# Kernel tuning notes

Hardware: AMD Instinct MI355X
Metric: run time of the kernel (lower is better)

The kernel has to match this reference:

```python
import jax, jax.numpy as jnp
import numpy as np

B, S, H = 32, 2048, 1024

def setup_inputs() -> dict:
    key = jax.random.key(0)
    ks = jax.random.split(key, 8)
    s = 1.0 / np.sqrt(H)
    return {
        "query": jax.random.normal(ks[0], (B, 1, H), jnp.float32),
        "keys": jax.random.normal(ks[1], (B, S, H), jnp.float32),
        "Wa_w": jax.random.normal(ks[2], (H, H), jnp.float32) * s,
        "Wa_b": jax.random.normal(ks[3], (H,), jnp.float32) * s,
        "Ua_w": jax.random.normal(ks[4], (H, H), jnp.float32) * s,
        "Ua_b": jax.random.normal(ks[5], (H,), jnp.float32) * s,
        "Va_w": jax.random.normal(ks[6], (1, H), jnp.float32) * s,
        "Va_b": jax.random.normal(ks[7], (1,), jnp.float32) * s,
    }

def reference(query, keys, Wa_w, Wa_b, Ua_w, Ua_b, Va_w, Va_b):
    # Wa(query): (B,1,H); Ua(keys): (B,S,H); broadcast add -> (B,S,H)
    q = jnp.einsum('bqh,oh->bqo', query, Wa_w) + Wa_b
    k = jnp.einsum('bsh,oh->bso', keys, Ua_w) + Ua_b
    h = jnp.tanh(q + k)                              # (B,S,H)
    scores = jnp.einsum('bsh,oh->bso', h, Va_w) + Va_b  # (B,S,1)
    scores = scores[:, :, 0][:, None, :]             # (B,1,S)
    weights = jax.nn.softmax(scores, axis=-1)        # (B,1,S)
    context = jnp.einsum('bqs,bsh->bqh', weights, keys)  # (B,1,H)
    return context, weights
```

## Files before the change

kernel.cpp:

```cpp
#include <hip/hip_runtime.h>
#include <hip/hip_bf16.h>

#define HDIM 1024
#define SEQ  2048
#define BATCH 32
#define M_TOTAL (BATCH * SEQ)
#define BM 128
#define BN 256
#define BK 64
#define NSLICE 8

typedef __bf16 bf16x8 __attribute__((ext_vector_type(8)));
typedef float  f32x4  __attribute__((ext_vector_type(4)));
typedef unsigned short u16;
#define AS1 __attribute__((address_space(1)))
#define AS3 __attribute__((address_space(3)))

__device__ __forceinline__ u16 f2bf(float f) {
    unsigned int u = __float_as_uint(f);
    u += 0x7FFFu + ((u >> 16) & 1u);
    return (u16)(u >> 16);
}

__global__ __launch_bounds__(256) void cvt_kernel(const float* __restrict__ in,
                                                  u16* __restrict__ out) {
    size_t i = ((size_t)blockIdx.x * 256 + threadIdx.x) * 8;
    float4 f0 = *(const float4*)(in + i);
    float4 f1 = *(const float4*)(in + i + 4);
    uint4 v;
    v.x = (unsigned)f2bf(f0.x) | ((unsigned)f2bf(f0.y) << 16);
    v.y = (unsigned)f2bf(f0.z) | ((unsigned)f2bf(f0.w) << 16);
    v.z = (unsigned)f2bf(f1.x) | ((unsigned)f2bf(f1.y) << 16);
    v.w = (unsigned)f2bf(f1.z) | ((unsigned)f2bf(f1.w) << 16);
    *(uint4*)(out + i) = v;
}

__global__ __launch_bounds__(256) void qb_kernel(const float* __restrict__ query,
                                                 const float* __restrict__ Wa_w,
                                                 const float* __restrict__ Wa_b,
                                                 const float* __restrict__ Ua_b,
                                                 float* __restrict__ qb) {
    __shared__ float qs[HDIM];
    const int b = blockIdx.x;
    const int tid = threadIdx.x;
    ((float4*)qs)[tid] = ((const float4*)(query + b * HDIM))[tid];
    __syncthreads();
    const int lane = tid & 63;
    const int w = tid >> 6;
    const int obase = blockIdx.y * 64 + w * 16;
    for (int i = 0; i < 16; i++) {
        int o = obase + i;
        const float4* wrow = (const float4*)(Wa_w + (size_t)o * HDIM);
        float s = 0.f;
        #pragma unroll
        for (int j = 0; j < 4; j++) {
            float4 wv = wrow[j * 64 + lane];
            float4 qv = ((const float4*)qs)[j * 64 + lane];
            s += wv.x * qv.x + wv.y * qv.y + wv.z * qv.z + wv.w * qv.w;
        }
        #pragma unroll
        for (int m = 1; m < 64; m <<= 1) s += __shfl_xor(s, m);
        if (lane == 0) qb[b * HDIM + o] = s + Wa_b[o] + Ua_b[o];
    }
}

__global__ __launch_bounds__(256, 2) void gemm_score_kernel(const u16* __restrict__ keysb,
                                                            const u16* __restrict__ uab,
                                                            const float* __restrict__ qb,
                                                            const float* __restrict__ vaw,
                                                            float* __restrict__ sp) {
    __shared__ __align__(16) u16 As[BM * BK];
    __shared__ __align__(16) u16 Bs[BN * BK];
    const int tid  = threadIdx.x;
    const int lane = tid & 63;
    const int w    = tid >> 6;
    const int n0 = blockIdx.x * BN;
    const int m0 = blockIdx.y * BM;
    const int wave_m = (w & 1) * 64;
    const int wave_n = (w >> 1) * 128;

    f32x4 acc[4][8] = {};

    const int srow = lane >> 3;
    const int scol = (lane & 7) * 8;
    const u16* gA = keysb + (size_t)(m0 + w * 32 + srow) * HDIM + scol;
    const u16* gB = uab   + (size_t)(n0 + w * 64 + srow) * HDIM + scol;
    u16* lA = As + (w * 32) * BK;
    u16* lB = Bs + (w * 64) * BK;

    const int fr = lane & 15;
    const int fq = lane >> 4;

    for (int k0 = 0; k0 < HDIM; k0 += BK) {
        __syncthreads();
        #pragma unroll
        for (int i = 0; i < 4; i++)
            __builtin_amdgcn_global_load_lds((AS1 void*)(gA + k0 + i * 8 * HDIM),
                                             (AS3 void*)(lA + i * 8 * BK), 16, 0, 0);
        #pragma unroll
        for (int i = 0; i < 8; i++)
            __builtin_amdgcn_global_load_lds((AS1 void*)(gB + k0 + i * 8 * HDIM),
                                             (AS3 void*)(lB + i * 8 * BK), 16, 0, 0);
        __syncthreads();

        #pragma unroll
        for (int j = 0; j < 2; j++) {
            bf16x8 a[4], b[8];
            #pragma unroll
            for (int i = 0; i < 4; i++)
                a[i] = *(const bf16x8*)(As + (wave_m + i * 16 + fr) * BK + j * 32 + fq * 8);
            #pragma unroll
            for (int i = 0; i < 8; i++)
                b[i] = *(const bf16x8*)(Bs + (wave_n + i * 16 + fr) * BK + j * 32 + fq * 8);
            #pragma unroll
            for (int mi = 0; mi < 4; mi++)
                #pragma unroll
                for (int ni = 0; ni < 8; ni++)
                    acc[mi][ni] = __builtin_amdgcn_mfma_f32_16x16x32_bf16(a[mi], b[ni], acc[mi][ni], 0, 0, 0);
        }
    }

    const int bidx = m0 >> 11;
    float qv[8], vv[8];
    #pragma unroll
    for (int ni = 0; ni < 8; ni++) {
        int n_g = n0 + wave_n + ni * 16 + fr;
        qv[ni] = qb[bidx * HDIM + n_g];
        vv[ni] = vaw[n_g];
    }
    const int slice = blockIdx.x * 2 + (w >> 1);
    float* sl = sp + ((size_t)slice * BATCH + bidx) * SEQ;
    #pragma unroll
    for (int mi = 0; mi < 4; mi++) {
        #pragma unroll
        for (int r = 0; r < 4; r++) {
            float p = 0.f;
            #pragma unroll
            for (int ni = 0; ni < 8; ni++) {
                float x = acc[mi][ni][r] + qv[ni];
                float e = __expf(2.f * x);
                p += (1.f - 2.f / (e + 1.f)) * vv[ni];
            }
            p += __shfl_xor(p, 1);
            p += __shfl_xor(p, 2);
            p += __shfl_xor(p, 4);
            p += __shfl_xor(p, 8);
            if (fr == 0) {
                int s_g = (m0 + wave_m + mi * 16 + fq * 4 + r) & (SEQ - 1);
                sl[s_g] = p;
            }
        }
    }
}

__global__ __launch_bounds__(256) void softmax_kernel(const float* __restrict__ sp,
                                                      float* __restrict__ weights,
                                                      float* __restrict__ ctx) {
    __shared__ float red[4];
    const int b = blockIdx.x;
    const int tid = threadIdx.x;
    float4 z = {0.f, 0.f, 0.f, 0.f};
    ((float4*)(ctx + b * HDIM))[tid] = z;
    float v[8];
    float mx = -1e30f;
    #pragma unroll
    for (int i = 0; i < 8; i++) {
        int s = tid + i * 256;
        float a = 0.f;
        #pragma unroll
        for (int j = 0; j < NSLICE; j++) a += sp[((size_t)j * BATCH + b) * SEQ + s];
        v[i] = a;
        mx = fmaxf(mx, a);
    }
    #pragma unroll
    for (int m = 1; m < 64; m <<= 1) mx = fmaxf(mx, __shfl_xor(mx, m));
    if ((tid & 63) == 0) red[tid >> 6] = mx;
    __syncthreads();
    mx = fmaxf(fmaxf(red[0], red[1]), fmaxf(red[2], red[3]));
    float sum = 0.f;
    #pragma unroll
    for (int i = 0; i < 8; i++) { v[i] = __expf(v[i] - mx); sum += v[i]; }
    #pragma unroll
    for (int m = 1; m < 64; m <<= 1) sum += __shfl_xor(sum, m);
    __syncthreads();
    if ((tid & 63) == 0) red[tid >> 6] = sum;
    __syncthreads();
    sum = red[0] + red[1] + red[2] + red[3];
    float inv = 1.f / sum;
    #pragma unroll
    for (int i = 0; i < 8; i++) weights[b * SEQ + tid + i * 256] = v[i] * inv;
}

__global__ __launch_bounds__(256) void context_kernel(const u16* __restrict__ keysb,
                                                      const float* __restrict__ weights,
                                                      float* __restrict__ ctx) {
    __shared__ float wsm[256];
    const int b = blockIdx.x;
    const int s0 = blockIdx.y * 256;
    const int tid = threadIdx.x;
    wsm[tid] = weights[b * SEQ + s0 + tid];
    __syncthreads();
    const int hq = tid & 127;
    const int sh = (tid >> 7) * 128;
    float a0 = 0.f, a1 = 0.f, a2 = 0.f, a3 = 0.f;
    float a4 = 0.f, a5 = 0.f, a6 = 0.f, a7 = 0.f;
    const uint4* kp = (const uint4*)(keysb + (size_t)b * SEQ * HDIM
                                     + (size_t)(s0 + sh) * HDIM) + hq;
    #pragma unroll 8
    for (int s = 0; s < 128; s++) {
        uint4 kv = kp[s * 128];
        float wv = wsm[sh + s];
        a0 += wv * __uint_as_float(kv.x << 16);
        a1 += wv * __uint_as_float(kv.x & 0xFFFF0000u);
        a2 += wv * __uint_as_float(kv.y << 16);
        a3 += wv * __uint_as_float(kv.y & 0xFFFF0000u);
        a4 += wv * __uint_as_float(kv.z << 16);
        a5 += wv * __uint_as_float(kv.z & 0xFFFF0000u);
        a6 += wv * __uint_as_float(kv.w << 16);
        a7 += wv * __uint_as_float(kv.w & 0xFFFF0000u);
    }
    float* o = ctx + b * HDIM + hq * 8;
    atomicAdd(o + 0, a0);
    atomicAdd(o + 1, a1);
    atomicAdd(o + 2, a2);
    atomicAdd(o + 3, a3);
    atomicAdd(o + 4, a4);
    atomicAdd(o + 5, a5);
    atomicAdd(o + 6, a6);
    atomicAdd(o + 7, a7);
}

extern "C" void kernel_launch(void* const* d_in, const int* in_sizes, int n_in,
                              void* d_out, int out_size, void* d_ws, size_t ws_size,
                              hipStream_t stream) {
    const float* query = (const float*)d_in[0];
    const float* keys  = (const float*)d_in[1];
    const float* Wa_w  = (const float*)d_in[2];
    const float* Wa_b  = (const float*)d_in[3];
    const float* Ua_w  = (const float*)d_in[4];
    const float* Ua_b  = (const float*)d_in[5];
    const float* Va_w  = (const float*)d_in[6];
    float* out = (float*)d_out;

    char* ws = (char*)d_ws;
    u16*  keysb = (u16*)ws;
    u16*  uab   = (u16*)(ws + 134217728);
    float* qb   = (float*)(ws + 134217728 + 2097152);
    float* sp   = (float*)(ws + 134217728 + 2097152 + 131072);

    cvt_kernel<<<(BATCH * SEQ * HDIM) / 2048, 256, 0, stream>>>(keys, keysb);
    cvt_kernel<<<(HDIM * HDIM) / 2048, 256, 0, stream>>>(Ua_w, uab);
    qb_kernel<<<dim3(BATCH, HDIM / 64), 256, 0, stream>>>(query, Wa_w, Wa_b, Ua_b, qb);
    gemm_score_kernel<<<dim3(HDIM / BN, M_TOTAL / BM), 256, 0, stream>>>(keysb, uab, qb, Va_w, sp);
    softmax_kernel<<<BATCH, 256, 0, stream>>>(sp, out + BATCH * HDIM, out);
    context_kernel<<<dim3(BATCH, 8), 256, 0, stream>>>(keysb, out + BATCH * HDIM, out);
}
```

Before: 623.0 us.

## Rework score GEMM into 256x256 tile with 4-stage LDS pipeline and swizzling

The bf16 score GEMM now uses 512-thread blocks computing 256x256 tiles with BK=32. A four-deep LDS ring is filled by direct global-to-LDS loads, with explicit vmcnt waits, barriers and raised MFMA priority so loads overlap compute. An XOR swizzle on LDS columns is meant to cut bank conflicts, and a block-index remap is meant to improve L2 reuse. The number of partial score slices grows to 16. The cost is about 128KB of LDS per block, which limits occupancy, plus hand-tuned waitcnt logic that is fragile.

```diff
diff --git a/kernel.cpp b/kernel.cpp
--- a/kernel.cpp
+++ b/kernel.cpp
@@ -5,10 +5,11 @@
 #define SEQ  2048
 #define BATCH 32
 #define M_TOTAL (BATCH * SEQ)
-#define BM 128
+#define BM 256
 #define BN 256
-#define BK 64
-#define NSLICE 8
+#define BK 32
+#define KSTEPS (HDIM / BK)
+#define NSLICE 16
 
 typedef __bf16 bf16x8 __attribute__((ext_vector_type(8)));
 typedef float  f32x4  __attribute__((ext_vector_type(4)));
@@ -64,79 +65,115 @@
     }
 }
 
-__global__ __launch_bounds__(256, 2) void gemm_score_kernel(const u16* __restrict__ keysb,
+__global__ __launch_bounds__(512, 2) void gemm_score_kernel(const u16* __restrict__ keysb,
                                                             const u16* __restrict__ uab,
                                                             const float* __restrict__ qb,
                                                             const float* __restrict__ vaw,
                                                             float* __restrict__ sp) {
-    __shared__ __align__(16) u16 As[BM * BK];
-    __shared__ __align__(16) u16 Bs[BN * BK];
+    __shared__ __align__(16) u16 As[4][BM * BK];
+    __shared__ __align__(16) u16 Bs[4][BN * BK];
+
     const int tid  = threadIdx.x;
     const int lane = tid & 63;
     const int w    = tid >> 6;
-    const int n0 = blockIdx.x * BN;
-    const int m0 = blockIdx.y * BM;
-    const int wave_m = (w & 1) * 64;
-    const int wave_n = (w >> 1) * 128;
-
-    f32x4 acc[4][8] = {};
-
-    const int srow = lane >> 3;
-    const int scol = (lane & 7) * 8;
-    const u16* gA = keysb + (size_t)(m0 + w * 32 + srow) * HDIM + scol;
-    const u16* gB = uab   + (size_t)(n0 + w * 64 + srow) * HDIM + scol;
-    u16* lA = As + (w * 32) * BK;
-    u16* lB = Bs + (w * 64) * BK;
+    const int wm   = w >> 2;
+    const int wn   = w & 3;
+
+    const int bid = blockIdx.y * 4 + blockIdx.x;
+    const int swz = (bid & 7) * 128 + (bid >> 3);
+    const int bx  = swz & 3;
+    const int by  = swz >> 2;
+    const int n0  = bx * BN;
+    const int m0  = by * BM;
+
+    const int srow = lane >> 2;
+    const int cs   = (lane & 3) ^ ((lane >> 3) & 3);
+    const u16* gA0 = keysb + (size_t)(m0 + w * 32 + srow) * HDIM + cs * 8;
+    const u16* gB0 = uab   + (size_t)(n0 + w * 32 + srow) * HDIM + cs * 8;
+    const int ldst = w * 32 * BK;
 
     const int fr = lane & 15;
     const int fq = lane >> 4;
-
-    for (int k0 = 0; k0 < HDIM; k0 += BK) {
-        __syncthreads();
-        #pragma unroll
-        for (int i = 0; i < 4; i++)
-            __builtin_amdgcn_global_load_lds((AS1 void*)(gA + k0 + i * 8 * HDIM),
-                                             (AS3 void*)(lA + i * 8 * BK), 16, 0, 0);
-        #pragma unroll
-        for (int i = 0; i < 8; i++)
-            __builtin_amdgcn_global_load_lds((AS1 void*)(gB + k0 + i * 8 * HDIM),
-                                             (AS3 void*)(lB + i * 8 * BK), 16, 0, 0);
-        __syncthreads();
-
-        #pragma unroll
-        for (int j = 0; j < 2; j++) {
-            bf16x8 a[4], b[8];
+    const int sA = fq ^ ((fr >> 1) & 3);
+    const int aoff = (wm * 128 + fr) * BK + sA * 8;
+    const int boff = (wn * 64  + fr) * BK + sA * 8;
+
+    f32x4 acc[8][4] = {};
+
+#define STAGE_A(kt) { \
+    u16* d = &As[(kt) & 3][ldst]; \
+    __builtin_amdgcn_global_load_lds((AS1 void*)(gA0 + (size_t)(kt) * BK), (AS3 void*)d, 16, 0, 0); \
+    __builtin_amdgcn_global_load_lds((AS1 void*)(gA0 + (size_t)(kt) * BK + 16 * HDIM), (AS3 void*)(d + 16 * BK), 16, 0, 0); }
+#define STAGE_B(kt) { \
+    u16* d = &Bs[(kt) & 3][ldst]; \
+    __builtin_amdgcn_global_load_lds((AS1 void*)(gB0 + (size_t)(kt) * BK), (AS3 void*)d, 16, 0, 0); \
+    __builtin_amdgcn_global_load_lds((AS1 void*)(gB0 + (size_t)(kt) * BK + 16 * HDIM), (AS3 void*)(d + 16 * BK), 16, 0, 0); }
+
+    STAGE_A(0) STAGE_B(0)
+    STAGE_A(1) STAGE_B(1)
+    STAGE_A(2) STAGE_B(2)
+
+    for (int t = 0; t < KSTEPS; ++t) {
+        if (t < KSTEPS - 2)       asm volatile("s_waitcnt vmcnt(8)" ::: "memory");
+        else if (t == KSTEPS - 2) asm volatile("s_waitcnt vmcnt(4)" ::: "memory");
+        else                      asm volatile("s_waitcnt vmcnt(0)" ::: "memory");
+        __builtin_amdgcn_s_barrier();
+
+        const u16* ap = &As[t & 3][aoff];
+        const u16* bp = &Bs[t & 3][boff];
+        bf16x8 a[8], b[4];
+
+        #pragma unroll
+        for (int i = 0; i < 4; i++) a[i] = *(const bf16x8*)(ap + i * 16 * BK);
+        #pragma unroll
+        for (int i = 0; i < 4; i++) b[i] = *(const bf16x8*)(bp + i * 16 * BK);
+        if (t + 3 < KSTEPS) STAGE_A(t + 3)
+        __builtin_amdgcn_s_barrier();
+        asm volatile("s_waitcnt lgkmcnt(0)" ::: "memory");
+        __builtin_amdgcn_sched_barrier(0);
+        __builtin_amdgcn_s_setprio(1);
+        #pragma unroll
+        for (int mi = 0; mi < 4; mi++)
             #pragma unroll
-            for (int i = 0; i < 4; i++)
-                a[i] = *(const bf16x8*)(As + (wave_m + i * 16 + fr) * BK + j * 32 + fq * 8);
+            for (int ni = 0; ni < 4; ni++)
+                acc[mi][ni] = __builtin_amdgcn_mfma_f32_16x16x32_bf16(a[mi], b[ni], acc[mi][ni], 0, 0, 0);
+        __builtin_amdgcn_s_setprio(0);
+        __builtin_amdgcn_s_barrier();
+
+        #pragma unroll
+        for (int i = 4; i < 8; i++) a[i] = *(const bf16x8*)(ap + i * 16 * BK);
+        if (t + 3 < KSTEPS) STAGE_B(t + 3)
+        __builtin_amdgcn_s_barrier();
+        asm volatile("s_waitcnt lgkmcnt(0)" ::: "memory");
+        __builtin_amdgcn_sched_barrier(0);
+        __builtin_amdgcn_s_setprio(1);
+        #pragma unroll
+        for (int mi = 4; mi < 8; mi++)
             #pragma unroll
-            for (int i = 0; i < 8; i++)
-                b[i] = *(const bf16x8*)(Bs + (wave_n + i * 16 + fr) * BK + j * 32 + fq * 8);
-            #pragma unroll
-            for (int mi = 0; mi < 4; mi++)
-                #pragma unroll
-                for (int ni = 0; ni < 8; ni++)
-                    acc[mi][ni] = __builtin_amdgcn_mfma_f32_16x16x32_bf16(a[mi], b[ni], acc[mi][ni], 0, 0, 0);
-        }
-    }
+            for (int ni = 0; ni < 4; ni++)
+                acc[mi][ni] = __builtin_amdgcn_mfma_f32_16x16x32_bf16(a[mi], b[ni], acc[mi][ni], 0, 0, 0);
+        __builtin_amdgcn_s_setprio(0);
+    }
+#undef STAGE_A
+#undef STAGE_B
 
     const int bidx = m0 >> 11;
-    float qv[8], vv[8];
-    #pragma unroll
-    for (int ni = 0; ni < 8; ni++) {
-        int n_g = n0 + wave_n + ni * 16 + fr;
+    float qv[4], vv[4];
+    #pragma unroll
+    for (int ni = 0; ni < 4; ni++) {
+        int n_g = n0 + wn * 64 + ni * 16 + fr;
         qv[ni] = qb[bidx * HDIM + n_g];
         vv[ni] = vaw[n_g];
     }
-    const int slice = blockIdx.x * 2 + (w >> 1);
+    const int slice = bx * 4 + wn;
     float* sl = sp + ((size_t)slice * BATCH + bidx) * SEQ;
     #pragma unroll
-    for (int mi = 0; mi < 4; mi++) {
+    for (int mi = 0; mi < 8; mi++) {
         #pragma unroll
         for (int r = 0; r < 4; r++) {
             float p = 0.f;
             #pragma unroll
-            for (int ni = 0; ni < 8; ni++) {
+            for (int ni = 0; ni < 4; ni++) {
                 float x = acc[mi][ni][r] + qv[ni];
                 float e = __expf(2.f * x);
                 p += (1.f - 2.f / (e + 1.f)) * vv[ni];
@@ -146,7 +183,7 @@
             p += __shfl_xor(p, 4);
             p += __shfl_xor(p, 8);
             if (fr == 0) {
-                int s_g = (m0 + wave_m + mi * 16 + fq * 4 + r) & (SEQ - 1);
+                int s_g = (m0 + wm * 128 + mi * 16 + fq * 4 + r) & (SEQ - 1);
                 sl[s_g] = p;
             }
         }
@@ -251,7 +288,7 @@
     cvt_kernel<<<(BATCH * SEQ * HDIM) / 2048, 256, 0, stream>>>(keys, keysb);
     cvt_kernel<<<(HDIM * HDIM) / 2048, 256, 0, stream>>>(Ua_w, uab);
     qb_kernel<<<dim3(BATCH, HDIM / 64), 256, 0, stream>>>(query, Wa_w, Wa_b, Ua_b, qb);
-    gemm_score_kernel<<<dim3(HDIM / BN, M_TOTAL / BM), 256, 0, stream>>>(keysb, uab, qb, Va_w, sp);
+    gemm_score_kernel<<<dim3(HDIM / BN, M_TOTAL / BM), 512, 0, stream>>>(keysb, uab, qb, Va_w, sp);
     softmax_kernel<<<BATCH, 256, 0, stream>>>(sp, out + BATCH * HDIM, out);
     context_kernel<<<dim3(BATCH, 8), 256, 0, stream>>>(keysb, out + BATCH * HDIM, out);
 }
```

Measured after the change: 629.8 us. No clear change (+1.1%).
